# Optimization experiments

Measured on AMD Instinct MI355X. Metric: run time of the kernel, lower is better.

Reference implementation:

```python
import jax, jax.numpy as jnp
import numpy as np

N, F_IN, C, H, E, G = 10000, 128, 256, 4, 160000, 512
BN_EPS = 1e-5


def setup_inputs() -> dict:
    key = jax.random.key(0)
    ks = iter(jax.random.split(key, 40))
    nrm = lambda shape, s=0.05: jax.random.normal(next(ks), shape, jnp.float32) * s

    def bn(dim):
        # rows: gamma, beta, running_mean, running_var (eval-mode BatchNorm)
        g = 1.0 + jax.random.normal(next(ks), (dim,), jnp.float32) * 0.1
        b = jax.random.normal(next(ks), (dim,), jnp.float32) * 0.1
        m = jax.random.normal(next(ks), (dim,), jnp.float32) * 0.1
        v = jax.random.uniform(next(ks), (dim,), jnp.float32, 0.5, 1.5)
        return jnp.stack([g, b, m, v])  # [4, dim]

    x = jax.random.normal(next(ks), (N, F_IN), jnp.float32)
    edge_index = jax.random.randint(next(ks), (2, E), 0, N, jnp.int64)
    batch = (jnp.arange(N, dtype=jnp.int64) * G) // N  # sorted, every graph non-empty

    return {
        "x": x, "edge_index": edge_index, "batch": batch,
        "W1": nrm((F_IN, H * C)), "att_src1": nrm((H, C)), "att_dst1": nrm((H, C)), "b1": nrm((H * C,)), "bn1": bn(H * C),
        "W2": nrm((H * C, H * C)), "att_src2": nrm((H, C)), "att_dst2": nrm((H, C)), "b2": nrm((H * C,)), "bn2": bn(H * C),
        "W3": nrm((H * C, C)), "att_src3": nrm((1, C)), "att_dst3": nrm((1, C)), "b3": nrm((C,)), "bn3": bn(C),
        "fc1_w": nrm((3 * C, 2 * C)), "fc1_b": nrm((2 * C,)), "bnf1": bn(2 * C),
        "fc2_w": nrm((2 * C, C)), "fc2_b": nrm((C,)), "bnf2": bn(C),
        "fc3_w": nrm((C, 1)), "fc3_b": nrm((1,)),
    }


def batchnorm(x, p):
    g, b, m, v = p
    return (x - m) * (g * jax.lax.rsqrt(v + BN_EPS)) + b


def gat_conv(x, src, dst, W, att_src, att_dst, bias, heads):
    n = x.shape[0]
    h = (x @ W).reshape(n, heads, -1)                      # [N,H,C]
    a_src = jnp.einsum('nhc,hc->nh', h, att_src)           # [N,H]
    a_dst = jnp.einsum('nhc,hc->nh', h, att_dst)
    logits = jax.nn.leaky_relu(a_src[src] + a_dst[dst], 0.2)  # [E,H]
    # scatter-softmax over incoming edges of each destination node
    m = jax.ops.segment_max(logits, dst, num_segments=n)
    m = jax.lax.stop_gradient(jnp.where(jnp.isfinite(m), m, 0.0))
    e = jnp.exp(logits - m[dst])
    denom = jax.ops.segment_sum(e, dst, num_segments=n)
    alpha = e / (denom[dst] + 1e-16)                       # [E,H]
    msg = h[src] * alpha[:, :, None]                       # [E,H,C]
    out = jax.ops.segment_sum(msg, dst, num_segments=n)    # [N,H,C]
    return out.reshape(n, -1) + bias


def reference(x, edge_index, batch,
              W1, att_src1, att_dst1, b1, bn1,
              W2, att_src2, att_dst2, b2, bn2,
              W3, att_src3, att_dst3, b3, bn3,
              fc1_w, fc1_b, bnf1, fc2_w, fc2_b, bnf2, fc3_w, fc3_b):
    src, dst = edge_index[0], edge_index[1]
    h = jax.nn.elu(batchnorm(gat_conv(x, src, dst, W1, att_src1, att_dst1, b1, H), bn1))
    h = jax.nn.elu(batchnorm(gat_conv(h, src, dst, W2, att_src2, att_dst2, b2, H), bn2))
    h = jax.nn.elu(batchnorm(gat_conv(h, src, dst, W3, att_src3, att_dst3, b3, 1), bn3))
    # multi-pool readout over graphs
    s = jax.ops.segment_sum(h, batch, num_segments=G)
    cnt = jax.ops.segment_sum(jnp.ones((h.shape[0], 1), h.dtype), batch, num_segments=G)
    mean = s / cnt
    mx = jax.ops.segment_max(h, batch, num_segments=G)
    z = jnp.concatenate([mean, mx, s], axis=1)             # [G, 3C]
    z = jax.nn.relu(batchnorm(z @ fc1_w + fc1_b, bnf1))    # dropout: eval mode (identity)
    z = jax.nn.relu(batchnorm(z @ fc2_w + fc2_b, bnf2))
    return z @ fc3_w + fc3_b                               # [G, 1]
```

## Files before the change

kernel.cpp:

```cpp
#include <hip/hip_runtime.h>
#include <math.h>

#define N_NODES 10000
#define N_EDGES 160000
#define N_GRAPH 512

#define NEG_INF (-1e30f)

typedef __attribute__((ext_vector_type(8))) short s16x8;
typedef __attribute__((ext_vector_type(4))) float f32x4;

__device__ __forceinline__ unsigned short f2b(float f) {
  union { float f; unsigned u; } c{f};
  unsigned u = c.u;
  return (unsigned short)((u + 0x7fff + ((u >> 16) & 1)) >> 16);
}
__device__ __forceinline__ float b2f(unsigned short h) {
  union { unsigned u; float f; } c{(unsigned)h << 16};
  return c.f;
}
__device__ __forceinline__ void up2(unsigned d, float& lo, float& hi) {
  union { unsigned u; float f; } a{d << 16}, b{d & 0xffff0000u};
  lo = a.f; hi = b.f;
}
__device__ __forceinline__ float lrelu(float x) { return x > 0.f ? x : 0.2f * x; }

#define GLL16(gp, lp)                                                          \
  __builtin_amdgcn_global_load_lds(                                            \
      (const __attribute__((address_space(1))) unsigned int*)(gp),             \
      (__attribute__((address_space(3))) unsigned int*)(lp), 16, 0, 0)

__global__ void k_count(const int* __restrict__ dst, const int* __restrict__ batch,
                        int* __restrict__ deg, int* __restrict__ gcnt) {
  int i = blockIdx.x * 256 + threadIdx.x;
  if (i < N_EDGES) atomicAdd(&deg[dst[i]], 1);
  if (i < N_NODES) atomicAdd(&gcnt[batch[i]], 1);
}

__global__ void k_scan(const int* __restrict__ in, int* __restrict__ out, int n) {
  __shared__ int buf[1024];
  __shared__ int carry_s;
  if (threadIdx.x == 0) carry_s = 0;
  __syncthreads();
  for (int base = 0; base < n; base += 1024) {
    int i = base + (int)threadIdx.x;
    int v = (i < n) ? in[i] : 0;
    buf[threadIdx.x] = v;
    __syncthreads();
    for (int off = 1; off < 1024; off <<= 1) {
      int t = (threadIdx.x >= (unsigned)off) ? buf[threadIdx.x - off] : 0;
      __syncthreads();
      buf[threadIdx.x] += t;
      __syncthreads();
    }
    int carry = carry_s;
    if (i < n) out[i] = carry + buf[threadIdx.x] - v;
    __syncthreads();
    if (threadIdx.x == 0) carry_s = carry + buf[1023];
    __syncthreads();
  }
  if (threadIdx.x == 0) out[n] = carry_s;
}

__global__ void k_fill(const int* __restrict__ src, const int* __restrict__ dst,
                       const int* __restrict__ rowoff, int* __restrict__ cursor,
                       int* __restrict__ csr) {
  int e = blockIdx.x * 256 + threadIdx.x;
  if (e < N_EDGES) {
    int d = dst[e];
    int p = atomicAdd(&cursor[d], 1);
    csr[rowoff[d] + p] = src[e];
  }
}

__global__ __launch_bounds__(256) void k_sortseg(const int* __restrict__ rowoff,
                                                 int* __restrict__ vals) {
  const int node = blockIdx.x * 4 + (threadIdx.x >> 6);
  if (node >= N_NODES) return;
  const int lane = threadIdx.x & 63;
  const int a = rowoff[node], b = rowoff[node + 1];
  const int deg = b - a;
  if (deg <= 1) return;
  if (deg <= 64) {
    int v = (lane < deg) ? vals[a + lane] : 0x7fffffff;
#pragma unroll
    for (int ph = 0; ph < 64; ++ph) {
      const int par = ph & 1;
      const bool left = ((lane & 1) == par);
      const int partner = left ? lane + 1 : lane - 1;
      const int pv = __shfl(v, partner & 63);
      if (partner >= 0 && partner < 64) v = left ? min(v, pv) : max(v, pv);
    }
    if (lane < deg) vals[a + lane] = v;
  } else if (lane == 0) {
    for (int p = a + 1; p < b; ++p) {
      int v = vals[p];
      int q = p - 1;
      while (q >= a && vals[q] > v) { vals[q + 1] = vals[q]; --q; }
      vals[q + 1] = v;
    }
  }
}

__global__ void k_f2b4(const float* __restrict__ in, unsigned short* __restrict__ out, int n4) {
  int i = blockIdx.x * 256 + threadIdx.x;
  if (i < n4) {
    float4 v = ((const float4*)in)[i];
    ushort4 o;
    o.x = f2b(v.x); o.y = f2b(v.y); o.z = f2b(v.z); o.w = f2b(v.w);
    ((ushort4*)out)[i] = o;
  }
}

__global__ __launch_bounds__(256) void k_convT(const float* __restrict__ in,
                                               unsigned short* __restrict__ out,
                                               int K, int M) {
  __shared__ float t[32][33];
  const int mb = blockIdx.x * 32, kb = blockIdx.y * 32;
  const int tx = threadIdx.x & 31, ty = threadIdx.x >> 5;
#pragma unroll
  for (int r = ty; r < 32; r += 8) t[r][tx] = in[(size_t)(kb + r) * M + mb + tx];
  __syncthreads();
#pragma unroll
  for (int r = ty; r < 32; r += 8)
    out[(size_t)(mb + r) * K + kb + tx] = f2b(t[tx][r]);
}

__global__ __launch_bounds__(256) void k_gemm_bf16(
    const unsigned short* __restrict__ A, const unsigned short* __restrict__ Bt,
    unsigned short* __restrict__ Cbf, int M, int N, int K) {
  __shared__ unsigned short As[128 * 32];
  __shared__ unsigned short Bs[128 * 32];
  const int tid = threadIdx.x;
  const int lane = tid & 63, wave = tid >> 6;
  const int wr = wave >> 1, wc = wave & 1;
  const int m0 = blockIdx.y * 128, n0 = blockIdx.x * 128;

  f32x4 acc[4][4];
#pragma unroll
  for (int i = 0; i < 4; ++i)
#pragma unroll
    for (int j = 0; j < 4; ++j) acc[i][j] = (f32x4){0.f, 0.f, 0.f, 0.f};

  const int l4 = lane >> 2;
  const int kp8 = (lane & 3) * 8;
  int rA0 = m0 + wave * 32 + l4;
  int rA1 = rA0 + 16;
  rA0 = min(rA0, M - 1);
  rA1 = min(rA1, M - 1);
  const int rB0 = n0 + wave * 32 + l4;
  const int rB1 = rB0 + 16;
  const unsigned short* pA0 = A + (size_t)rA0 * K + kp8;
  const unsigned short* pA1 = A + (size_t)rA1 * K + kp8;
  const unsigned short* pB0 = Bt + (size_t)rB0 * K + kp8;
  const unsigned short* pB1 = Bt + (size_t)rB1 * K + kp8;
  unsigned short* lA = As + wave * 1024;
  unsigned short* lB = Bs + wave * 1024;

  const int fr = lane & 15, kg = (lane >> 4) * 8;

  for (int kb = 0; kb < K; kb += 32) {
    GLL16(pA0 + kb, lA);
    GLL16(pA1 + kb, lA + 512);
    GLL16(pB0 + kb, lB);
    GLL16(pB1 + kb, lB + 512);
    __syncthreads();

    s16x8 a[4], b[4];
#pragma unroll
    for (int m = 0; m < 4; ++m)
      a[m] = *(const s16x8*)&As[(wr * 64 + m * 16 + fr) * 32 + kg];
#pragma unroll
    for (int n = 0; n < 4; ++n)
      b[n] = *(const s16x8*)&Bs[(wc * 64 + n * 16 + fr) * 32 + kg];
#pragma unroll
    for (int m = 0; m < 4; ++m)
#pragma unroll
      for (int n = 0; n < 4; ++n)
        acc[m][n] = __builtin_amdgcn_mfma_f32_16x16x32_bf16(a[m], b[n], acc[m][n], 0, 0, 0);
    __syncthreads();
  }

  const int frow = (lane >> 4) * 4;
#pragma unroll
  for (int m = 0; m < 4; ++m) {
#pragma unroll
    for (int r = 0; r < 4; ++r) {
      const int row = m0 + wr * 64 + m * 16 + frow + r;
      if (row < M) {
#pragma unroll
        for (int n = 0; n < 4; ++n) {
          const int col = n0 + wc * 64 + n * 16 + fr;
          Cbf[(size_t)row * N + col] = f2b(acc[m][n][r]);
        }
      }
    }
  }
}

template <int K, int M>
__global__ __launch_bounds__(256) void k_head_fc(
    const float* __restrict__ A, const float* __restrict__ W,
    float* __restrict__ C, const float* __restrict__ bias,
    const float* __restrict__ bn) {
  constexpr int KQ = K / 4;
  __shared__ float Ap[8 * K];
  __shared__ float part[4][8][64];
  const int tid = threadIdx.x;
  const int g0 = blockIdx.y * 8;
  const int m0 = blockIdx.x * 64;
  const int c = tid & 63;
  const int q = tid >> 6;

  for (int i = tid; i < 8 * K / 4; i += 256)
    ((float4*)Ap)[i] = ((const float4*)(A + (size_t)g0 * K))[i];
  __syncthreads();

  float acc[8];
#pragma unroll
  for (int r = 0; r < 8; ++r) acc[r] = 0.f;

  const float* Wc = W + m0 + c;
  const int k0 = q * KQ;
  for (int k = k0; k < k0 + KQ; k += 4) {
    float wv[4];
#pragma unroll
    for (int u = 0; u < 4; ++u) wv[u] = Wc[(size_t)(k + u) * M];
#pragma unroll
    for (int r = 0; r < 8; ++r) {
      const float4 a4 = *(const float4*)&Ap[r * K + k];
      acc[r] += a4.x * wv[0] + a4.y * wv[1] + a4.z * wv[2] + a4.w * wv[3];
    }
  }

#pragma unroll
  for (int r = 0; r < 8; ++r) part[q][r][c] = acc[r];
  __syncthreads();

  for (int i = tid; i < 512; i += 256) {
    const int r = i >> 6, cc = i & 63;
    float v = part[0][r][cc] + part[1][r][cc] + part[2][r][cc] + part[3][r][cc];
    const int gc = m0 + cc;
    v += bias[gc];
    const float g = bn[gc], b = bn[M + gc], mu = bn[2 * M + gc], var = bn[3 * M + gc];
    v = (v - mu) * (g * rsqrtf(var + 1e-5f)) + b;
    v = fmaxf(v, 0.f);
    C[(size_t)(g0 + r) * M + gc] = v;
  }
}

template <int HEADS>
__global__ __launch_bounds__(256) void k_att(const unsigned short* __restrict__ h,
                                             const float* __restrict__ att_s,
                                             const float* __restrict__ att_d,
                                             float* __restrict__ aS,
                                             float* __restrict__ aD) {
  const int pair = blockIdx.x * 4 + (threadIdx.x >> 6);
  if (pair >= N_NODES * HEADS) return;
  const int node = pair / HEADS, hd = pair % HEADS;
  const int lane = threadIdx.x & 63;
  const unsigned short* row = h + (size_t)node * HEADS * 256 + hd * 256;
  const ushort4 v = *(const ushort4*)&row[lane * 4];
  const float4 s4 = *(const float4*)&att_s[hd * 256 + lane * 4];
  const float4 d4 = *(const float4*)&att_d[hd * 256 + lane * 4];
  float ss = b2f(v.x) * s4.x + b2f(v.y) * s4.y + b2f(v.z) * s4.z + b2f(v.w) * s4.w;
  float sd = b2f(v.x) * d4.x + b2f(v.y) * d4.y + b2f(v.z) * d4.z + b2f(v.w) * d4.w;
#pragma unroll
  for (int off = 32; off; off >>= 1) {
    ss += __shfl_xor(ss, off);
    sd += __shfl_xor(sd, off);
  }
  if (lane == 0) {
    aS[pair] = ss;
    aD[pair] = sd;
  }
}

__global__ __launch_bounds__(256) void k_aggw4(
    const unsigned short* __restrict__ hpre, const float* __restrict__ aS,
    const float* __restrict__ aD, const int* __restrict__ rowoff,
    const int* __restrict__ csr, const float* __restrict__ bias,
    const float* __restrict__ bn, unsigned short* __restrict__ outb) {
  const int wv = threadIdx.x >> 6;
  const int lane = threadIdx.x & 63;
  const int node = blockIdx.x * 2 + (wv >> 1);
  const int half = wv & 1;
  if (node >= N_NODES) return;

  __shared__ int s_src_all[4][64];
  __shared__ float s_alp_all[4][64][2];
  int* s_src = s_src_all[wv];
  float (*s_alp)[2] = s_alp_all[wv];

  const int r0 = rowoff[node];
  const int deg = rowoff[node + 1] - r0;
  const float2 ad2 = *(const float2*)&aD[(size_t)node * 4 + half * 2];

  float acc[8];
#pragma unroll
  for (int j = 0; j < 8; ++j) acc[j] = 0.f;

  const int hg = lane >> 5;
  const size_t choff = (size_t)half * 512;

  auto gather = [&](int cnt) {
    int e = 0;
    for (; e + 4 <= cnt; e += 4) {
      uint4 v[4];
      float al[4];
#pragma unroll
      for (int u = 0; u < 4; ++u) {
        const int s = s_src[e + u];
        al[u] = s_alp[e + u][hg];
        v[u] = ((const uint4*)(hpre + ((size_t)s << 10) + choff))[lane];
      }
#pragma unroll
      for (int u = 0; u < 4; ++u) {
        float lo, hi;
        up2(v[u].x, lo, hi); acc[0] += al[u] * lo; acc[1] += al[u] * hi;
        up2(v[u].y, lo, hi); acc[2] += al[u] * lo; acc[3] += al[u] * hi;
        up2(v[u].z, lo, hi); acc[4] += al[u] * lo; acc[5] += al[u] * hi;
        up2(v[u].w, lo, hi); acc[6] += al[u] * lo; acc[7] += al[u] * hi;
      }
    }
    for (; e < cnt; ++e) {
      const int s = s_src[e];
      const float al = s_alp[e][hg];
      const uint4 v = ((const uint4*)(hpre + ((size_t)s << 10) + choff))[lane];
      float lo, hi;
      up2(v.x, lo, hi); acc[0] += al * lo; acc[1] += al * hi;
      up2(v.y, lo, hi); acc[2] += al * lo; acc[3] += al * hi;
      up2(v.z, lo, hi); acc[4] += al * lo; acc[5] += al * hi;
      up2(v.w, lo, hi); acc[6] += al * lo; acc[7] += al * hi;
    }
  };

  if (deg <= 64) {
    float la, lb;
    int sE = 0;
    const bool act = lane < deg;
    if (act) {
      sE = csr[r0 + lane];
      const float2 sv = *(const float2*)&aS[(size_t)sE * 4 + half * 2];
      la = lrelu(sv.x + ad2.x);
      lb = lrelu(sv.y + ad2.y);
    } else {
      la = lb = NEG_INF;
    }
    float ma = la, mb = lb;
#pragma unroll
    for (int off = 32; off; off >>= 1) {
      ma = fmaxf(ma, __shfl_xor(ma, off));
      mb = fmaxf(mb, __shfl_xor(mb, off));
    }
    float ea = act ? __expf(la - ma) : 0.f;
    float eb = act ? __expf(lb - mb) : 0.f;
    float sa = ea, sb = eb;
#pragma unroll
    for (int off = 32; off; off >>= 1) {
      sa += __shfl_xor(sa, off);
      sb += __shfl_xor(sb, off);
    }
    if (act) {
      s_src[lane] = sE;
      s_alp[lane][0] = ea / (sa + 1e-16f);
      s_alp[lane][1] = eb / (sb + 1e-16f);
    }
    gather(deg);
  } else {
    auto logits = [&](int idx, float& a, float& b, int& s) {
      s = csr[r0 + idx];
      const float2 sv = *(const float2*)&aS[(size_t)s * 4 + half * 2];
      a = lrelu(sv.x + ad2.x);
      b = lrelu(sv.y + ad2.y);
    };
    float ma = NEG_INF, mb = NEG_INF;
    for (int base = 0; base < deg; base += 64) {
      if (base + lane < deg) {
        float a, b; int s;
        logits(base + lane, a, b, s);
        ma = fmaxf(ma, a); mb = fmaxf(mb, b);
      }
    }
#pragma unroll
    for (int off = 32; off; off >>= 1) {
      ma = fmaxf(ma, __shfl_xor(ma, off));
      mb = fmaxf(mb, __shfl_xor(mb, off));
    }
    float sa = 0.f, sb = 0.f;
    for (int base = 0; base < deg; base += 64) {
      if (base + lane < deg) {
        float a, b; int s;
        logits(base + lane, a, b, s);
        sa += __expf(a - ma); sb += __expf(b - mb);
      }
    }
#pragma unroll
    for (int off = 32; off; off >>= 1) {
      sa += __shfl_xor(sa, off);
      sb += __shfl_xor(sb, off);
    }
    const float da = 1.f / (sa + 1e-16f), db = 1.f / (sb + 1e-16f);
    for (int base = 0; base < deg; base += 64) {
      const int cnt = min(64, deg - base);
      if (lane < cnt) {
        float a, b; int s;
        logits(base + lane, a, b, s);
        s_src[lane] = s;
        s_alp[lane][0] = __expf(a - ma) * da;
        s_alp[lane][1] = __expf(b - mb) * db;
      }
      gather(cnt);
    }
  }

  const int cb = half * 512 + lane * 8;
  unsigned od[4];
#pragma unroll
  for (int jj = 0; jj < 2; ++jj) {
    const float4 bi = *(const float4*)&bias[cb + jj * 4];
    const float4 gg = *(const float4*)&bn[cb + jj * 4];
    const float4 bb = *(const float4*)&bn[1024 + cb + jj * 4];
    const float4 mm = *(const float4*)&bn[2048 + cb + jj * 4];
    const float4 vv = *(const float4*)&bn[3072 + cb + jj * 4];
    float r[4];
#pragma unroll
    for (int j = 0; j < 4; ++j) {
      float v = acc[jj * 4 + j] + ((const float*)&bi)[j];
      v = (v - ((const float*)&mm)[j]) *
              (((const float*)&gg)[j] * rsqrtf(((const float*)&vv)[j] + 1e-5f)) +
          ((const float*)&bb)[j];
      v = v > 0.f ? v : (__expf(v) - 1.f);
      r[j] = v;
    }
    od[jj * 2 + 0] = (unsigned)f2b(r[0]) | ((unsigned)f2b(r[1]) << 16);
    od[jj * 2 + 1] = (unsigned)f2b(r[2]) | ((unsigned)f2b(r[3]) << 16);
  }
  *(uint4*)&outb[((size_t)node << 10) + cb] = make_uint4(od[0], od[1], od[2], od[3]);
}

__global__ __launch_bounds__(256) void k_aggw1(
    const unsigned short* __restrict__ hpre, const float* __restrict__ aS,
    const float* __restrict__ aD, const int* __restrict__ rowoff,
    const int* __restrict__ csr, const float* __restrict__ bias,
    const float* __restrict__ bn, float* __restrict__ outf) {
  const int wv = threadIdx.x >> 6;
  const int lane = threadIdx.x & 63;
  const int node = blockIdx.x * 4 + wv;
  if (node >= N_NODES) return;

  __shared__ int s_src_all[4][64];
  __shared__ float s_alp_all[4][64];
  int* s_src = s_src_all[wv];
  float* s_alp = s_alp_all[wv];

  const int r0 = rowoff[node];
  const int deg = rowoff[node + 1] - r0;
  const float ad = aD[node];

  float acc[4] = {0.f, 0.f, 0.f, 0.f};

  auto gather = [&](int cnt) {
    int e = 0;
    for (; e + 4 <= cnt; e += 4) {
      uint2 v[4];
      float al[4];
#pragma unroll
      for (int u = 0; u < 4; ++u) {
        const int s = s_src[e + u];
        al[u] = s_alp[e + u];
        v[u] = ((const uint2*)(hpre + ((size_t)s << 8)))[lane];
      }
#pragma unroll
      for (int u = 0; u < 4; ++u) {
        float lo, hi;
        up2(v[u].x, lo, hi); acc[0] += al[u] * lo; acc[1] += al[u] * hi;
        up2(v[u].y, lo, hi); acc[2] += al[u] * lo; acc[3] += al[u] * hi;
      }
    }
    for (; e < cnt; ++e) {
      const int s = s_src[e];
      const float al = s_alp[e];
      const uint2 v = ((const uint2*)(hpre + ((size_t)s << 8)))[lane];
      float lo, hi;
      up2(v.x, lo, hi); acc[0] += al * lo; acc[1] += al * hi;
      up2(v.y, lo, hi); acc[2] += al * lo; acc[3] += al * hi;
    }
  };

  if (deg <= 64) {
    float l0;
    int sE = 0;
    const bool act = lane < deg;
    if (act) {
      sE = csr[r0 + lane];
      l0 = lrelu(aS[sE] + ad);
    } else {
      l0 = NEG_INF;
    }
    float m0 = l0;
#pragma unroll
    for (int off = 32; off; off >>= 1) m0 = fmaxf(m0, __shfl_xor(m0, off));
    float e0 = act ? __expf(l0 - m0) : 0.f;
    float s0 = e0;
#pragma unroll
    for (int off = 32; off; off >>= 1) s0 += __shfl_xor(s0, off);
    if (act) {
      s_src[lane] = sE;
      s_alp[lane] = e0 / (s0 + 1e-16f);
    }
    gather(deg);
  } else {
    float m0 = NEG_INF;
    for (int base = 0; base < deg; base += 64)
      if (base + lane < deg) m0 = fmaxf(m0, lrelu(aS[csr[r0 + base + lane]] + ad));
#pragma unroll
    for (int off = 32; off; off >>= 1) m0 = fmaxf(m0, __shfl_xor(m0, off));
    float s0 = 0.f;
    for (int base = 0; base < deg; base += 64)
      if (base + lane < deg) s0 += __expf(lrelu(aS[csr[r0 + base + lane]] + ad) - m0);
#pragma unroll
    for (int off = 32; off; off >>= 1) s0 += __shfl_xor(s0, off);
    const float d0 = 1.f / (s0 + 1e-16f);
    for (int base = 0; base < deg; base += 64) {
      const int cnt = min(64, deg - base);
      if (lane < cnt) {
        const int s = csr[r0 + base + lane];
        s_src[lane] = s;
        s_alp[lane] = __expf(lrelu(aS[s] + ad) - m0) * d0;
      }
      gather(cnt);
    }
  }

  const int c = lane * 4;
  const float4 bi = *(const float4*)&bias[c];
  const float4 gg = *(const float4*)&bn[c];
  const float4 bb = *(const float4*)&bn[256 + c];
  const float4 mm = *(const float4*)&bn[512 + c];
  const float4 vv = *(const float4*)&bn[768 + c];
  float4 o;
#pragma unroll
  for (int j = 0; j < 4; ++j) {
    float v = acc[j] + ((const float*)&bi)[j];
    v = (v - ((const float*)&mm)[j]) *
            (((const float*)&gg)[j] * rsqrtf(((const float*)&vv)[j] + 1e-5f)) +
        ((const float*)&bb)[j];
    v = v > 0.f ? v : (__expf(v) - 1.f);
    ((float*)&o)[j] = v;
  }
  *(float4*)&outf[((size_t)node << 8) + c] = o;
}

__global__ __launch_bounds__(256) void k_pool(const float* __restrict__ h,
                                              const int* __restrict__ goff,
                                              float* __restrict__ z) {
  const int g = blockIdx.x;
  const int c = threadIdx.x;
  const int i0 = goff[g], i1 = goff[g + 1];
  float s = 0.f, mx = NEG_INF;
  for (int i = i0; i < i1; ++i) {
    float v = h[(size_t)i * 256 + c];
    s += v;
    mx = fmaxf(mx, v);
  }
  const float cnt = (float)(i1 - i0);
  z[(size_t)g * 768 + c] = s / cnt;
  z[(size_t)g * 768 + 256 + c] = mx;
  z[(size_t)g * 768 + 512 + c] = s;
}

__global__ __launch_bounds__(64) void k_fc3(const float* __restrict__ z2,
                                            const float* __restrict__ w,
                                            const float* __restrict__ b,
                                            float* __restrict__ out) {
  const int g = blockIdx.x;
  const int lane = threadIdx.x;
  float s = 0.f;
#pragma unroll
  for (int j = 0; j < 4; ++j) {
    int c = lane + 64 * j;
    s += z2[(size_t)g * 256 + c] * w[c];
  }
#pragma unroll
  for (int off = 32; off; off >>= 1) s += __shfl_xor(s, off);
  if (lane == 0) out[g] = s + b[0];
}

extern "C" void kernel_launch(void* const* d_in, const int* in_sizes, int n_in,
                              void* d_out, int out_size, void* d_ws, size_t ws_size,
                              hipStream_t stream) {
  const float* x    = (const float*)d_in[0];
  const int* ei     = (const int*)d_in[1];
  const int* batch  = (const int*)d_in[2];
  const float* W1   = (const float*)d_in[3];
  const float* as1  = (const float*)d_in[4];
  const float* ad1  = (const float*)d_in[5];
  const float* b1   = (const float*)d_in[6];
  const float* bn1  = (const float*)d_in[7];
  const float* W2   = (const float*)d_in[8];
  const float* as2  = (const float*)d_in[9];
  const float* ad2  = (const float*)d_in[10];
  const float* b2   = (const float*)d_in[11];
  const float* bn2  = (const float*)d_in[12];
  const float* W3   = (const float*)d_in[13];
  const float* as3  = (const float*)d_in[14];
  const float* ad3  = (const float*)d_in[15];
  const float* b3   = (const float*)d_in[16];
  const float* bn3  = (const float*)d_in[17];
  const float* fc1w = (const float*)d_in[18];
  const float* fc1b = (const float*)d_in[19];
  const float* bnf1 = (const float*)d_in[20];
  const float* fc2w = (const float*)d_in[21];
  const float* fc2b = (const float*)d_in[22];
  const float* bnf2 = (const float*)d_in[23];
  const float* fc3w = (const float*)d_in[24];
  const float* fc3b = (const float*)d_in[25];
  float* out = (float*)d_out;

  const int* e_src = ei;
  const int* e_dst = ei + N_EDGES;

  char* w = (char*)d_ws;
  auto alloc = [&](size_t bytes) -> void* {
    void* p = (void*)w;
    w += (bytes + 255) & ~(size_t)255;
    return p;
  };
  unsigned short* x_bf  = (unsigned short*)alloc((size_t)N_NODES * 128 * 2);
  unsigned short* W1t   = (unsigned short*)alloc((size_t)1024 * 128 * 2);
  unsigned short* W2t   = (unsigned short*)alloc((size_t)1024 * 1024 * 2);
  unsigned short* W3t   = (unsigned short*)alloc((size_t)256 * 1024 * 2);
  unsigned short* hA_bf = (unsigned short*)alloc((size_t)N_NODES * 1024 * 2);
  unsigned short* hB_bf = (unsigned short*)alloc((size_t)N_NODES * 1024 * 2);
  float* hB_f32 = (float*)alloc((size_t)N_NODES * 256 * 4);
  float* aS   = (float*)alloc((size_t)N_NODES * 4 * 4);
  float* aD   = (float*)alloc((size_t)N_NODES * 4 * 4);
  int* deg    = (int*)alloc((size_t)(2 * N_NODES + N_GRAPH) * 4);
  int* cursor = deg + N_NODES;
  int* gcnt   = deg + 2 * N_NODES;
  int* rowoff = (int*)alloc((size_t)(N_NODES + 1) * 4);
  int* goff   = (int*)alloc((size_t)(N_GRAPH + 1) * 4);
  int* csr    = (int*)alloc((size_t)N_EDGES * 4);
  float* z    = (float*)alloc((size_t)N_GRAPH * 768 * 4);
  float* z1   = (float*)alloc((size_t)N_GRAPH * 512 * 4);
  float* z2   = (float*)alloc((size_t)N_GRAPH * 256 * 4);

  hipMemsetAsync(deg, 0, (size_t)(2 * N_NODES + N_GRAPH) * 4, stream);

  k_f2b4<<<(N_NODES * 128 / 4 + 255) / 256, 256, 0, stream>>>(x, x_bf, N_NODES * 128 / 4);
  k_convT<<<dim3(1024 / 32, 128 / 32), 256, 0, stream>>>(W1, W1t, 128, 1024);
  k_convT<<<dim3(1024 / 32, 1024 / 32), 256, 0, stream>>>(W2, W2t, 1024, 1024);
  k_convT<<<dim3(256 / 32, 1024 / 32), 256, 0, stream>>>(W3, W3t, 1024, 256);

  k_count<<<(N_EDGES + 255) / 256, 256, 0, stream>>>(e_dst, batch, deg, gcnt);
  k_scan<<<1, 1024, 0, stream>>>(deg, rowoff, N_NODES);
  k_scan<<<1, 1024, 0, stream>>>(gcnt, goff, N_GRAPH);
  k_fill<<<(N_EDGES + 255) / 256, 256, 0, stream>>>(e_src, e_dst, rowoff, cursor, csr);
  k_sortseg<<<(N_NODES + 3) / 4, 256, 0, stream>>>(rowoff, csr);

  const int mt = (N_NODES + 127) / 128;
  const int nb2 = (N_NODES + 1) / 2;
  const int nb4 = (N_NODES + 3) / 4;

  k_gemm_bf16<<<dim3(1024 / 128, mt), 256, 0, stream>>>(x_bf, W1t, hA_bf, N_NODES, 1024, 128);
  k_att<4><<<(N_NODES * 4 + 3) / 4, 256, 0, stream>>>(hA_bf, as1, ad1, aS, aD);
  k_aggw4<<<nb2, 256, 0, stream>>>(hA_bf, aS, aD, rowoff, csr, b1, bn1, hB_bf);

  k_gemm_bf16<<<dim3(1024 / 128, mt), 256, 0, stream>>>(hB_bf, W2t, hA_bf, N_NODES, 1024, 1024);
  k_att<4><<<(N_NODES * 4 + 3) / 4, 256, 0, stream>>>(hA_bf, as2, ad2, aS, aD);
  k_aggw4<<<nb2, 256, 0, stream>>>(hA_bf, aS, aD, rowoff, csr, b2, bn2, hB_bf);

  k_gemm_bf16<<<dim3(256 / 128, mt), 256, 0, stream>>>(hB_bf, W3t, hA_bf, N_NODES, 256, 1024);
  k_att<1><<<(N_NODES + 3) / 4, 256, 0, stream>>>(hA_bf, as3, ad3, aS, aD);
  k_aggw1<<<nb4, 256, 0, stream>>>(hA_bf, aS, aD, rowoff, csr, b3, bn3, hB_f32);

  k_pool<<<N_GRAPH, 256, 0, stream>>>(hB_f32, goff, z);
  k_head_fc<768, 512><<<dim3(512 / 64, N_GRAPH / 8), 256, 0, stream>>>(z, fc1w, z1, fc1b, bnf1);
  k_head_fc<512, 256><<<dim3(256 / 64, N_GRAPH / 8), 256, 0, stream>>>(z1, fc2w, z2, fc2b, bnf2);
  k_fc3<<<N_GRAPH, 64, 0, stream>>>(z2, fc3w, fc3b, out);
}
```

Before: 314.3 us.

## Reorder first GAT layer to aggregate raw inputs before projection

For layer 1, attention scores are computed directly from x using precomputed W1·att vectors. Softmax-weighted aggregation then runs on the 128-wide input features per head, producing a 512-wide tensor instead of gathering 1024-wide projected features. Four per-head GEMMs follow, with bias, batchnorm and ELU fused into their epilogue. This replaces gathering over 1024-wide rows with 128-wide rows and drops separate attention and aggregation passes. It adds an extra intermediate buffer, four smaller GEMM launches, and fp32 logits taken from x rather than from bf16-rounded h.

```diff
diff --git a/kernel.cpp b/kernel.cpp
--- a/kernel.cpp
+++ b/kernel.cpp
@@ -126,9 +126,238 @@
     out[(size_t)(mb + r) * K + kb + tx] = f2b(t[tx][r]);
 }
 
+__global__ void k_wmix(const float* __restrict__ W, const float* __restrict__ attS,
+                       const float* __restrict__ attD, float* __restrict__ wS,
+                       float* __restrict__ wD) {
+  const int i = blockIdx.x * 256 + threadIdx.x;
+  if (i >= 512) return;
+  const int f = i >> 2, h = i & 3;
+  const float* wrow = W + (size_t)f * 1024 + h * 256;
+  const float* as = attS + h * 256;
+  const float* ad = attD + h * 256;
+  float s = 0.f, d = 0.f;
+  for (int c = 0; c < 256; ++c) {
+    const float w = wrow[c];
+    s += w * as[c];
+    d += w * ad[c];
+  }
+  wS[f * 4 + h] = s;
+  wD[f * 4 + h] = d;
+}
+
+__global__ __launch_bounds__(256) void k_attx(const float* __restrict__ x,
+                                              const float* __restrict__ wS,
+                                              const float* __restrict__ wD,
+                                              float* __restrict__ aS,
+                                              float* __restrict__ aD) {
+  __shared__ float sS[128][4], sD[128][4];
+  const int tid = threadIdx.x;
+  for (int i = tid; i < 512; i += 256) {
+    sS[i >> 2][i & 3] = wS[i];
+    sD[i >> 2][i & 3] = wD[i];
+  }
+  __syncthreads();
+  const int node = blockIdx.x * 4 + (tid >> 6);
+  if (node >= N_NODES) return;
+  const int lane = tid & 63;
+  const float2 xv = ((const float2*)(x + (size_t)node * 128))[lane];
+  const float4 s0 = *(const float4*)sS[lane * 2];
+  const float4 s1 = *(const float4*)sS[lane * 2 + 1];
+  const float4 d0 = *(const float4*)sD[lane * 2];
+  const float4 d1 = *(const float4*)sD[lane * 2 + 1];
+  float a0 = xv.x * s0.x + xv.y * s1.x;
+  float a1 = xv.x * s0.y + xv.y * s1.y;
+  float a2 = xv.x * s0.z + xv.y * s1.z;
+  float a3 = xv.x * s0.w + xv.y * s1.w;
+  float b0 = xv.x * d0.x + xv.y * d1.x;
+  float b1 = xv.x * d0.y + xv.y * d1.y;
+  float b2 = xv.x * d0.z + xv.y * d1.z;
+  float b3 = xv.x * d0.w + xv.y * d1.w;
+#pragma unroll
+  for (int off = 32; off; off >>= 1) {
+    a0 += __shfl_xor(a0, off); a1 += __shfl_xor(a1, off);
+    a2 += __shfl_xor(a2, off); a3 += __shfl_xor(a3, off);
+    b0 += __shfl_xor(b0, off); b1 += __shfl_xor(b1, off);
+    b2 += __shfl_xor(b2, off); b3 += __shfl_xor(b3, off);
+  }
+  if (lane == 0) {
+    float4* pa = (float4*)&aS[(size_t)node * 4];
+    float4* pb = (float4*)&aD[(size_t)node * 4];
+    *pa = make_float4(a0, a1, a2, a3);
+    *pb = make_float4(b0, b1, b2, b3);
+  }
+}
+
+__global__ __launch_bounds__(256) void k_aggx(
+    const unsigned short* __restrict__ x_bf, const float* __restrict__ aS,
+    const float* __restrict__ aD, const int* __restrict__ rowoff,
+    const int* __restrict__ csr, unsigned short* __restrict__ xt) {
+  const int wv = threadIdx.x >> 6;
+  const int lane = threadIdx.x & 63;
+  const int node = blockIdx.x * 4 + wv;
+  if (node >= N_NODES) return;
+
+  __shared__ int s_src_all[4][64];
+  __shared__ float s_alp_all[4][64][4];
+  int* s_src = s_src_all[wv];
+  float (*s_alp)[4] = s_alp_all[wv];
+
+  const int r0 = rowoff[node];
+  const int deg = rowoff[node + 1] - r0;
+  const float4 ad4 = *(const float4*)&aD[(size_t)node * 4];
+
+  float acc[8];
+#pragma unroll
+  for (int j = 0; j < 8; ++j) acc[j] = 0.f;
+
+  auto gather = [&](int cnt) {
+    int e = 0;
+    for (; e + 4 <= cnt; e += 4) {
+      unsigned v[4];
+      float4 al[4];
+#pragma unroll
+      for (int u = 0; u < 4; ++u) {
+        const int s = s_src[e + u];
+        al[u] = *(const float4*)s_alp[e + u];
+        v[u] = ((const unsigned*)(x_bf + ((size_t)s << 7)))[lane];
+      }
+#pragma unroll
+      for (int u = 0; u < 4; ++u) {
+        float lo, hi;
+        up2(v[u], lo, hi);
+        acc[0] += al[u].x * lo; acc[1] += al[u].x * hi;
+        acc[2] += al[u].y * lo; acc[3] += al[u].y * hi;
+        acc[4] += al[u].z * lo; acc[5] += al[u].z * hi;
+        acc[6] += al[u].w * lo; acc[7] += al[u].w * hi;
+      }
+    }
+    for (; e < cnt; ++e) {
+      const int s = s_src[e];
+      const float4 al = *(const float4*)s_alp[e];
+      const unsigned v = ((const unsigned*)(x_bf + ((size_t)s << 7)))[lane];
+      float lo, hi;
+      up2(v, lo, hi);
+      acc[0] += al.x * lo; acc[1] += al.x * hi;
+      acc[2] += al.y * lo; acc[3] += al.y * hi;
+      acc[4] += al.z * lo; acc[5] += al.z * hi;
+      acc[6] += al.w * lo; acc[7] += al.w * hi;
+    }
+  };
+
+  if (deg <= 64) {
+    float l0, l1, l2, l3;
+    int sE = 0;
+    const bool act = lane < deg;
+    if (act) {
+      sE = csr[r0 + lane];
+      const float4 sv = *(const float4*)&aS[(size_t)sE * 4];
+      l0 = lrelu(sv.x + ad4.x);
+      l1 = lrelu(sv.y + ad4.y);
+      l2 = lrelu(sv.z + ad4.z);
+      l3 = lrelu(sv.w + ad4.w);
+    } else {
+      l0 = l1 = l2 = l3 = NEG_INF;
+    }
+    float m0 = l0, m1 = l1, m2 = l2, m3 = l3;
+#pragma unroll
+    for (int off = 32; off; off >>= 1) {
+      m0 = fmaxf(m0, __shfl_xor(m0, off));
+      m1 = fmaxf(m1, __shfl_xor(m1, off));
+      m2 = fmaxf(m2, __shfl_xor(m2, off));
+      m3 = fmaxf(m3, __shfl_xor(m3, off));
+    }
+    float e0 = act ? __expf(l0 - m0) : 0.f;
+    float e1 = act ? __expf(l1 - m1) : 0.f;
+    float e2 = act ? __expf(l2 - m2) : 0.f;
+    float e3 = act ? __expf(l3 - m3) : 0.f;
+    float s0 = e0, s1 = e1, s2 = e2, s3 = e3;
+#pragma unroll
+    for (int off = 32; off; off >>= 1) {
+      s0 += __shfl_xor(s0, off);
+      s1 += __shfl_xor(s1, off);
+      s2 += __shfl_xor(s2, off);
+      s3 += __shfl_xor(s3, off);
+    }
+    if (act) {
+      s_src[lane] = sE;
+      s_alp[lane][0] = e0 / (s0 + 1e-16f);
+      s_alp[lane][1] = e1 / (s1 + 1e-16f);
+      s_alp[lane][2] = e2 / (s2 + 1e-16f);
+      s_alp[lane][3] = e3 / (s3 + 1e-16f);
+    }
+    gather(deg);
+  } else {
+    auto logits = [&](int idx, float& a, float& b, float& c, float& d, int& s) {
+      s = csr[r0 + idx];
+      const float4 sv = *(const float4*)&aS[(size_t)s * 4];
+      a = lrelu(sv.x + ad4.x);
+      b = lrelu(sv.y + ad4.y);
+      c = lrelu(sv.z + ad4.z);
+      d = lrelu(sv.w + ad4.w);
+    };
+    float m0 = NEG_INF, m1 = NEG_INF, m2 = NEG_INF, m3 = NEG_INF;
+    for (int base = 0; base < deg; base += 64) {
+      if (base + lane < deg) {
+        float a, b, c, d; int s;
+        logits(base + lane, a, b, c, d, s);
+        m0 = fmaxf(m0, a); m1 = fmaxf(m1, b); m2 = fmaxf(m2, c); m3 = fmaxf(m3, d);
+      }
+    }
+#pragma unroll
+    for (int off = 32; off; off >>= 1) {
+      m0 = fmaxf(m0, __shfl_xor(m0, off));
+      m1 = fmaxf(m1, __shfl_xor(m1, off));
+      m2 = fmaxf(m2, __shfl_xor(m2, off));
+      m3 = fmaxf(m3, __shfl_xor(m3, off));
+    }
+    float s0 = 0.f, s1 = 0.f, s2 = 0.f, s3 = 0.f;
+    for (int base = 0; base < deg; base += 64) {
+      if (base + lane < deg) {
+        float a, b, c, d; int s;
+        logits(base + lane, a, b, c, d, s);
+        s0 += __expf(a - m0); s1 += __expf(b - m1);
+        s2 += __expf(c - m2); s3 += __expf(d - m3);
+      }
+    }
+#pragma unroll
+    for (int off = 32; off; off >>= 1) {
+      s0 += __shfl_xor(s0, off);
+      s1 += __shfl_xor(s1, off);
+      s2 += __shfl_xor(s2, off);
+      s3 += __shfl_xor(s3, off);
+    }
+    const float d0 = 1.f / (s0 + 1e-16f), d1 = 1.f / (s1 + 1e-16f);
+    const float d2 = 1.f / (s2 + 1e-16f), d3 = 1.f / (s3 + 1e-16f);
+    for (int base = 0; base < deg; base += 64) {
+      const int cnt = min(64, deg - base);
+      if (lane < cnt) {
+        float a, b, c, d; int s;
+        logits(base + lane, a, b, c, d, s);
+        s_src[lane] = s;
+        s_alp[lane][0] = __expf(a - m0) * d0;
+        s_alp[lane][1] = __expf(b - m1) * d1;
+        s_alp[lane][2] = __expf(c - m2) * d2;
+        s_alp[lane][3] = __expf(d - m3) * d3;
+      }
+      gather(cnt);
+    }
+  }
+
+#pragma unroll
+  for (int h = 0; h < 4; ++h) {
+    const unsigned o = (unsigned)f2b(acc[h * 2]) | ((unsigned)f2b(acc[h * 2 + 1]) << 16);
+    ((unsigned*)xt)[(size_t)node * 256 + h * 64 + lane] = o;
+  }
+}
+
+template <int EPI>
 __global__ __launch_bounds__(256) void k_gemm_bf16(
-    const unsigned short* __restrict__ A, const unsigned short* __restrict__ Bt,
-    unsigned short* __restrict__ Cbf, int M, int N, int K) {
+    const unsigned short* __restrict__ A, int lda,
+    const unsigned short* __restrict__ Bt, int ldb,
+    unsigned short* __restrict__ Cbf, int ldc,
+    int M, int N, int K,
+    const float* __restrict__ bias, const float* __restrict__ bn, int bnN,
+    int colofs) {
   __shared__ unsigned short As[128 * 32];
   __shared__ unsigned short Bs[128 * 32];
   const int tid = threadIdx.x;
@@ -150,10 +379,10 @@
   rA1 = min(rA1, M - 1);
   const int rB0 = n0 + wave * 32 + l4;
   const int rB1 = rB0 + 16;
-  const unsigned short* pA0 = A + (size_t)rA0 * K + kp8;
-  const unsigned short* pA1 = A + (size_t)rA1 * K + kp8;
-  const unsigned short* pB0 = Bt + (size_t)rB0 * K + kp8;
-  const unsigned short* pB1 = Bt + (size_t)rB1 * K + kp8;
+  const unsigned short* pA0 = A + (size_t)rA0 * lda + kp8;
+  const unsigned short* pA1 = A + (size_t)rA1 * lda + kp8;
+  const unsigned short* pB0 = Bt + (size_t)rB0 * ldb + kp8;
+  const unsigned short* pB1 = Bt + (size_t)rB1 * ldb + kp8;
   unsigned short* lA = As + wave * 1024;
   unsigned short* lB = Bs + wave * 1024;
 
@@ -191,7 +420,16 @@
 #pragma unroll
         for (int n = 0; n < 4; ++n) {
           const int col = n0 + wc * 64 + n * 16 + fr;
-          Cbf[(size_t)row * N + col] = f2b(acc[m][n][r]);
+          const int gcol = colofs + col;
+          float v = acc[m][n][r];
+          if (EPI == 1) {
+            v += bias[gcol];
+            const float g = bn[gcol], b = bn[bnN + gcol];
+            const float mu = bn[2 * bnN + gcol], var = bn[3 * bnN + gcol];
+            v = (v - mu) * (g * rsqrtf(var + 1e-5f)) + b;
+            v = v > 0.f ? v : (__expf(v) - 1.f);
+          }
+          Cbf[(size_t)row * ldc + gcol] = f2b(v);
         }
       }
     }
@@ -628,6 +866,7 @@
     return p;
   };
   unsigned short* x_bf  = (unsigned short*)alloc((size_t)N_NODES * 128 * 2);
+  unsigned short* xt    = (unsigned short*)alloc((size_t)N_NODES * 512 * 2);
   unsigned short* W1t   = (unsigned short*)alloc((size_t)1024 * 128 * 2);
   unsigned short* W2t   = (unsigned short*)alloc((size_t)1024 * 1024 * 2);
   unsigned short* W3t   = (unsigned short*)alloc((size_t)256 * 1024 * 2);
@@ -636,6 +875,8 @@
   float* hB_f32 = (float*)alloc((size_t)N_NODES * 256 * 4);
   float* aS   = (float*)alloc((size_t)N_NODES * 4 * 4);
   float* aD   = (float*)alloc((size_t)N_NODES * 4 * 4);
+  float* wS1  = (float*)alloc((size_t)512 * 4);
+  float* wD1  = (float*)alloc((size_t)512 * 4);
   int* deg    = (int*)alloc((size_t)(2 * N_NODES + N_GRAPH) * 4);
   int* cursor = deg + N_NODES;
   int* gcnt   = deg + 2 * N_NODES;
@@ -652,6 +893,8 @@
   k_convT<<<dim3(1024 / 32, 128 / 32), 256, 0, stream>>>(W1, W1t, 128, 1024);
   k_convT<<<dim3(1024 / 32, 1024 / 32), 256, 0, stream>>>(W2, W2t, 1024, 1024);
   k_convT<<<dim3(256 / 32, 1024 / 32), 256, 0, stream>>>(W3, W3t, 1024, 256);
+  k_wmix<<<2, 256, 0, stream>>>(W1, as1, ad1, wS1, wD1);
+  k_attx<<<(N_NODES + 3) / 4, 256, 0, stream>>>(x, wS1, wD1, aS, aD);
 
   k_count<<<(N_EDGES + 255) / 256, 256, 0, stream>>>(e_dst, batch, deg, gcnt);
   k_scan<<<1, 1024, 0, stream>>>(deg, rowoff, N_NODES);
@@ -663,15 +906,20 @@
   const int nb2 = (N_NODES + 1) / 2;
   const int nb4 = (N_NODES + 3) / 4;
 
-  k_gemm_bf16<<<dim3(1024 / 128, mt), 256, 0, stream>>>(x_bf, W1t, hA_bf, N_NODES, 1024, 128);
-  k_att<4><<<(N_NODES * 4 + 3) / 4, 256, 0, stream>>>(hA_bf, as1, ad1, aS, aD);
-  k_aggw4<<<nb2, 256, 0, stream>>>(hA_bf, aS, aD, rowoff, csr, b1, bn1, hB_bf);
-
-  k_gemm_bf16<<<dim3(1024 / 128, mt), 256, 0, stream>>>(hB_bf, W2t, hA_bf, N_NODES, 1024, 1024);
+  k_aggx<<<nb4, 256, 0, stream>>>(x_bf, aS, aD, rowoff, csr, xt);
+  for (int h = 0; h < 4; ++h) {
+    k_gemm_bf16<1><<<dim3(2, mt), 256, 0, stream>>>(
+        xt + h * 128, 512, W1t + (size_t)h * 256 * 128, 128, hB_bf, 1024,
+        N_NODES, 256, 128, b1, bn1, 1024, h * 256);
+  }
+
+  k_gemm_bf16<0><<<dim3(1024 / 128, mt), 256, 0, stream>>>(
+      hB_bf, 1024, W2t, 1024, hA_bf, 1024, N_NODES, 1024, 1024, nullptr, nullptr, 0, 0);
   k_att<4><<<(N_NODES * 4 + 3) / 4, 256, 0, stream>>>(hA_bf, as2, ad2, aS, aD);
   k_aggw4<<<nb2, 256, 0, stream>>>(hA_bf, aS, aD, rowoff, csr, b2, bn2, hB_bf);
 
-  k_gemm_bf16<<<dim3(256 / 128, mt), 256, 0, stream>>>(hB_bf, W3t, hA_bf, N_NODES, 256, 1024);
+  k_gemm_bf16<0><<<dim3(256 / 128, mt), 256, 0, stream>>>(
+      hB_bf, 1024, W3t, 1024, hA_bf, 256, N_NODES, 256, 1024, nullptr, nullptr, 0, 0);
   k_att<1><<<(N_NODES + 3) / 4, 256, 0, stream>>>(hA_bf, as3, ad3, aS, aD);
   k_aggw1<<<nb4, 256, 0, stream>>>(hA_bf, aS, aD, rowoff, csr, b3, bn3, hB_f32);
 
```

Result: slower. 341.9 us (+8.8%).
